# Performance work log

Measured on AMD Instinct MI355X. Metric: run time of the kernel, lower is better.

## Reference

```python
import jax, jax.numpy as jnp
import numpy as np


def reverse_padded(tokens, lengths):
    # reverse each row within its valid length; padding stays in place
    B, T = tokens.shape
    t = jnp.arange(T)[None, :]
    L = lengths[:, None]
    idx = jnp.where(t < L, L - 1 - t, t)
    return jnp.take_along_axis(tokens, idx, axis=1)


def lstm_layer(x, lengths, Wih, Whh, bih, bhh):
    # x: [T, B, I]; emulates packed LSTM: padded steps output zeros, state frozen
    T, B, _ = x.shape
    H = Whh.shape[1]
    xW = jnp.einsum('tbi,gi->tbg', x, Wih) + bih  # precompute input GEMM [T,B,4H]
    mask = (jnp.arange(T)[:, None] < lengths[None, :]).astype(x.dtype)[:, :, None]

    def step(carry, inp):
        h, c = carry
        xw, m = inp
        gates = xw + h @ Whh.T + bhh
        i, f, g, o = jnp.split(gates, 4, axis=-1)
        i = jax.nn.sigmoid(i); f = jax.nn.sigmoid(f)
        g = jnp.tanh(g); o = jax.nn.sigmoid(o)
        c_new = f * c + i * g
        h_new = o * jnp.tanh(c_new)
        h = m * h_new + (1.0 - m) * h
        c = m * c_new + (1.0 - m) * c
        return (h, c), m * h_new

    h0 = jnp.zeros((B, H), x.dtype)
    (hT, cT), out = jax.lax.scan(step, (h0, h0), (xW, mask))
    return out


def setup_inputs() -> dict:
    key = jax.random.key(0)
    ntoken, ninp, nhid, B, T = 50000, 512, 1024, 64, 512
    ks = jax.random.split(key, 40)
    inp = {}
    inp['input'] = jax.random.randint(ks[0], (B, T), 0, ntoken)
    lens = jnp.sort(jax.random.randint(ks[1], (B,), T // 4, T + 1))[::-1]
    inp['seq_lengths'] = lens.at[0].set(T)
    inp['enc'] = jax.random.uniform(ks[2], (ntoken, ninp), jnp.float32, -0.1, 0.1)
    k = 3
    for d in ('f', 'r'):
        for l in range(2):
            I = ninp if l == 0 else nhid
            s = 1.0 / np.sqrt(nhid)
            inp[f'Wih_{d}{l}'] = jax.random.uniform(ks[k], (4 * nhid, I), jnp.float32, -s, s); k += 1
            inp[f'Whh_{d}{l}'] = jax.random.uniform(ks[k], (4 * nhid, nhid), jnp.float32, -s, s); k += 1
            inp[f'bih_{d}{l}'] = jax.random.uniform(ks[k], (4 * nhid,), jnp.float32, -s, s); k += 1
            inp[f'bhh_{d}{l}'] = jax.random.uniform(ks[k], (4 * nhid,), jnp.float32, -s, s); k += 1
    return inp


def reference(input, seq_lengths, enc,
              Wih_f0, Whh_f0, bih_f0, bhh_f0,
              Wih_f1, Whh_f1, bih_f1, bhh_f1,
              Wih_r0, Whh_r0, bih_r0, bhh_r0,
              Wih_r1, Whh_r1, bih_r1, bhh_r1):
    # eval-mode Elmo forward (all dropouts identity)
    input_rev = reverse_padded(input, seq_lengths)
    emb = enc[input].transpose(1, 0, 2)          # [T,B,ninp]
    emb_rev = enc[input_rev].transpose(1, 0, 2)  # [T,B,ninp]
    h_f = lstm_layer(emb, seq_lengths, Wih_f0, Whh_f0, bih_f0, bhh_f0)
    h_f = lstm_layer(h_f, seq_lengths, Wih_f1, Whh_f1, bih_f1, bhh_f1)
    h_r = lstm_layer(emb_rev, seq_lengths, Wih_r0, Whh_r0, bih_r0, bhh_r0)
    h_r = lstm_layer(h_r, seq_lengths, Wih_r1, Whh_r1, bih_r1, bhh_r1)
    return jnp.concatenate([h_f, h_r], axis=-1)  # [T,B,2*nhid]
```

## Files before the change

kernel.cpp:

```cpp
#include <hip/hip_runtime.h>

#define TT 512
#define BB 64
#define NI 512
#define NH 1024
#define NG 4096

using bf16x8 = __attribute__((ext_vector_type(8))) __bf16;
using f32x4  = __attribute__((ext_vector_type(4))) float;

typedef __attribute__((address_space(3))) char       lds_char;
typedef const __attribute__((address_space(1))) char glb_char;

static __device__ __forceinline__ unsigned short f2bf(float f) {
  unsigned int u = __float_as_uint(f);
  u += 0x7fffu + ((u >> 16) & 1u);
  return (unsigned short)(u >> 16);
}

__global__ void prep_layer(const float* __restrict__ Wih, const float* __restrict__ Whh,
                           const float* __restrict__ bih, const float* __restrict__ bhh,
                           unsigned short* __restrict__ Wx, unsigned short* __restrict__ Wh,
                           float* __restrict__ bias, int Kx) {
  long nx = (long)NG * Kx;
  long nh = (long)NG * NH;
  long total = nx + nh + NG;
  for (long i = (long)blockIdx.x * blockDim.x + threadIdx.x; i < total;
       i += (long)gridDim.x * blockDim.x) {
    if (i < nx) {
      int p = (int)(i / Kx); int k = (int)(i - (long)p * Kx);
      int orig = (p & 3) * NH + (p >> 2);
      Wx[i] = f2bf(Wih[(long)orig * Kx + k]);
    } else if (i < nx + nh) {
      long j = i - nx;
      int p = (int)(j / NH); int k = (int)(j - (long)p * NH);
      int orig = (p & 3) * NH + (p >> 2);
      Wh[j] = f2bf(Whh[(long)orig * NH + k]);
    } else {
      int p = (int)(i - nx - nh);
      int orig = (p & 3) * NH + (p >> 2);
      bias[p] = bih[orig] + bhh[orig];
    }
  }
}

__global__ void prep_emb(const int* __restrict__ tok, const int* __restrict__ lens,
                         const float* __restrict__ enc,
                         unsigned short* __restrict__ embf, unsigned short* __restrict__ embr) {
  int row = blockIdx.x;
  int t = row / BB, b = row - (row / BB) * BB;
  int L = lens[b];
  int tf = tok[b * TT + t];
  int ir = (t < L) ? (L - 1 - t) : t;
  int tr_ = tok[b * TT + ir];
  int i = threadIdx.x;
  float4 vf = *(const float4*)(enc + (long)tf * NI + i * 4);
  float4 vr = *(const float4*)(enc + (long)tr_ * NI + i * 4);
  ushort4 of = make_ushort4(f2bf(vf.x), f2bf(vf.y), f2bf(vf.z), f2bf(vf.w));
  ushort4 orr = make_ushort4(f2bf(vr.x), f2bf(vr.y), f2bf(vr.z), f2bf(vr.w));
  *(ushort4*)(embf + (long)row * NI + i * 4) = of;
  *(ushort4*)(embr + (long)row * NI + i * 4) = orr;
}

struct KP {
  const int* lens;
  const unsigned short* emb[2];
  const unsigned short* Wx[4];
  const unsigned short* Wh[4];
  const float* bias[4];
  unsigned short* hist[4];
  unsigned int* slots;
  float* out;
};

static __device__ __forceinline__ void poll_comb(const unsigned int* slots, int g,
                                                 int v, int layer, int t) {
  const int lane = threadIdx.x & 63;
  const bool nown = (t > 0) && (lane < 8);
  const bool nprev = layer && (lane >= 8) && (lane < 16);
  const unsigned int* p = slots;
  unsigned tgt = 0u;
  if (nown)  { p = slots + (size_t)(g * 64 + v * 8 + lane) * 8;            tgt = (unsigned)t; }
  if (nprev) { p = slots + (size_t)((g - 1) * 64 + v * 8 + (lane - 8)) * 8; tgt = (unsigned)(t + 1); }
  for (;;) {
    unsigned val = __hip_atomic_load(p, __ATOMIC_RELAXED, __HIP_MEMORY_SCOPE_AGENT);
    if (__all((int)(val >= tgt))) break;
    __builtin_amdgcn_s_sleep(1);
  }
  asm volatile("" ::: "memory");
}

__global__ void __launch_bounds__(512, 2) lstm_main(KP P) {
  __shared__ f32x4 red[8 * 16 * 64];
  __shared__ unsigned short hrep[64][16];
  __shared__ float hrep2[64][17];
  const int tid = threadIdx.x, lane = tid & 63, wave = tid >> 6;
  const int v = wave;
  const int wg = blockIdx.x, g = wg >> 6, wl = wg & 63;
  const int dir = g >> 1, layer = g & 1;
  const int ln = lane & 15, kg = lane >> 4;

  bf16x8 wh[16], wx[16];
  const int row0 = wl * 64;
  {
    const unsigned short* Wh = P.Wh[g];
#pragma unroll
    for (int mt = 0; mt < 4; ++mt) {
      const unsigned short* p = Wh + (long)(row0 + mt * 16 + ln) * NH + v * 128 + kg * 8;
#pragma unroll
      for (int kk = 0; kk < 4; ++kk) wh[mt * 4 + kk] = *(const bf16x8*)(p + kk * 32);
    }
    const unsigned short* Wxp = P.Wx[g];
    if (layer) {
#pragma unroll
      for (int mt = 0; mt < 4; ++mt) {
        const unsigned short* p = Wxp + (long)(row0 + mt * 16 + ln) * NH + v * 128 + kg * 8;
#pragma unroll
        for (int kk = 0; kk < 4; ++kk) wx[mt * 4 + kk] = *(const bf16x8*)(p + kk * 32);
      }
    } else {
#pragma unroll
      for (int mt = 0; mt < 4; ++mt) {
        const unsigned short* p = Wxp + (long)(row0 + mt * 16 + ln) * NI + v * 64 + kg * 8;
#pragma unroll
        for (int kk = 0; kk < 2; ++kk) wx[mt * 2 + kk] = *(const bf16x8*)(p + kk * 32);
      }
#pragma unroll
      for (int i = 8; i < 16; ++i) wx[i] = (bf16x8)0;
    }
  }
#pragma unroll
  for (int i = 0; i < 16; ++i) {
    asm volatile("" : "+v"(reinterpret_cast<f32x4&>(wh[i])));
    asm volatile("" : "+v"(reinterpret_cast<f32x4&>(wx[i])));
  }

  unsigned short* hist = P.hist[g];
  const unsigned short* xprev = layer ? (const unsigned short*)P.hist[g - 1] : nullptr;
  const unsigned short* xemb = P.emb[dir];

  const int i0 = wave * 2;
  const int coll = (i0 >> 2) * 4 + kg;
  const int b0 = (i0 & 3) * 16 + ln;
  const int b1 = ((i0 + 1) & 3) * 16 + ln;
  const f32x4 bias_v = *(const f32x4*)(P.bias[g] + (wl * 16 + coll) * 4);
  const int L0 = P.lens[b0], L1 = P.lens[b1];
  float c0 = 0.f, c1 = 0.f;

  const int sr = wave * 8 + (lane >> 3);
  const int sc = lane & 7;

  lds_char* lslice = (lds_char*)((char*)red + v * 16384);

  for (int t = 0; t < TT; ++t) {
    f32x4 acc[16];
#pragma unroll
    for (int i = 0; i < 16; ++i) { f32x4 z = {0.f, 0.f, 0.f, 0.f}; acc[i] = z; }

    if (t > 0 || layer) poll_comb(P.slots, g, v, layer, t);

    if (t > 0) {
      const char* gsrc = (const char*)(hist + (size_t)(t - 1) * 65536 + (size_t)v * 8192);
#pragma unroll
      for (int c = 0; c < 16; ++c) {
        __builtin_amdgcn_global_load_lds(
            (glb_char*)(gsrc + c * 1024 + lane * 16),
            (lds_char*)(lslice + c * 1024), 16, 0, 0);
      }
    }

    if (layer) {
      const unsigned short* pb = xprev + (size_t)t * 65536 +
          (size_t)(v * 8 + (kg >> 1)) * 1024 + ln * 16 + (kg & 1) * 8;
      bf16x8 bx[4][4];
#pragma unroll
      for (int kk = 0; kk < 4; ++kk)
#pragma unroll
        for (int nt = 0; nt < 4; ++nt)
          bx[kk][nt] = *(const bf16x8*)(pb + kk * 2048 + nt * 256);
#pragma unroll
      for (int kk = 0; kk < 4; ++kk)
#pragma unroll
        for (int mt = 0; mt < 4; ++mt)
#pragma unroll
          for (int nt = 0; nt < 4; ++nt)
            acc[mt * 4 + nt] = __builtin_amdgcn_mfma_f32_16x16x32_bf16(
                wx[mt * 4 + kk], bx[kk][nt], acc[mt * 4 + nt], 0, 0, 0);
    } else {
      const unsigned short* pb = xemb + ((size_t)t * BB + ln) * NI + v * 64 + kg * 8;
      bf16x8 bx[2][4];
#pragma unroll
      for (int kk = 0; kk < 2; ++kk)
#pragma unroll
        for (int nt = 0; nt < 4; ++nt)
          bx[kk][nt] = *(const bf16x8*)(pb + kk * 32 + (size_t)nt * 16 * NI);
#pragma unroll
      for (int kk = 0; kk < 2; ++kk)
#pragma unroll
        for (int mt = 0; mt < 4; ++mt)
#pragma unroll
          for (int nt = 0; nt < 4; ++nt)
            acc[mt * 4 + nt] = __builtin_amdgcn_mfma_f32_16x16x32_bf16(
                wx[mt * 2 + kk], bx[kk][nt], acc[mt * 4 + nt], 0, 0, 0);
    }

    if (t > 0) {
      asm volatile("s_waitcnt vmcnt(0)" ::: "memory");
      __builtin_amdgcn_sched_barrier(0);
      const char* ls = (const char*)red + v * 16384 +
                       (kg >> 1) * 2048 + ln * 32 + (kg & 1) * 16;
      bf16x8 bh[2][4];
#pragma unroll
      for (int nt = 0; nt < 4; ++nt)
        bh[0][nt] = *(const bf16x8*)(ls + nt * 512);
#pragma unroll
      for (int kk = 0; kk < 4; ++kk) {
        if (kk < 3) {
#pragma unroll
          for (int nt = 0; nt < 4; ++nt)
            bh[(kk + 1) & 1][nt] = *(const bf16x8*)(ls + (kk + 1) * 4096 + nt * 512);
        }
#pragma unroll
        for (int mt = 0; mt < 4; ++mt)
#pragma unroll
          for (int nt = 0; nt < 4; ++nt)
            acc[mt * 4 + nt] = __builtin_amdgcn_mfma_f32_16x16x32_bf16(
                wh[mt * 4 + kk], bh[kk & 1][nt], acc[mt * 4 + nt], 0, 0, 0);
      }
      asm volatile("s_waitcnt lgkmcnt(0)" ::: "memory");
      __builtin_amdgcn_sched_barrier(0);
    }

#pragma unroll
    for (int i = 0; i < 16; ++i) red[(wave * 16 + i) * 64 + lane] = acc[i];
    __syncthreads();

#pragma unroll
    for (int u = 0; u < 2; ++u) {
      const int i = i0 + u;
      f32x4 gs = bias_v;
#pragma unroll
      for (int w2 = 0; w2 < 8; ++w2) gs += red[(w2 * 16 + i) * 64 + lane];
      float iv = 1.f / (1.f + __expf(-gs[0]));
      float fv = 1.f / (1.f + __expf(-gs[1]));
      float gv = 1.f - 2.f / (1.f + __expf(2.f * gs[2]));
      float og = 1.f / (1.f + __expf(-gs[3]));
      float cp = u ? c1 : c0;
      float cn = fv * cp + iv * gv;
      if (u) c1 = cn; else c0 = cn;
      float tc = 1.f - 2.f / (1.f + __expf(2.f * cn));
      float hn = og * tc;
      const int Lx = u ? L1 : L0;
      const int bx = u ? b1 : b0;
      float outv = (t < Lx) ? hn : 0.f;
      hrep[bx][coll] = f2bf(outv);
      if (layer) hrep2[bx][coll] = outv;
    }
    __syncthreads();

    {
      unsigned vv = ((const unsigned*)hrep)[tid];
      __hip_atomic_store(
          (unsigned*)(hist + (size_t)t * 65536 + (size_t)wl * 1024) + tid,
          vv, __ATOMIC_RELAXED, __HIP_MEMORY_SCOPE_AGENT);
    }
    asm volatile("s_waitcnt vmcnt(0)" ::: "memory");
    __syncthreads();
    if (tid == 0)
      __hip_atomic_store(P.slots + (size_t)wg * 8, (unsigned)(t + 1),
                         __ATOMIC_RELAXED, __HIP_MEMORY_SCOPE_AGENT);
    if (layer) {
#pragma unroll
      for (int u = 0; u < 2; ++u) {
        float vv = hrep2[sr][sc + u * 8];
        __builtin_nontemporal_store(
            vv, &P.out[(long)(t * BB + sr) * 2048 + dir * NH + wl * 16 + sc + u * 8]);
      }
    }
  }
}

extern "C" void kernel_launch(void* const* d_in, const int* in_sizes, int n_in,
                              void* d_out, int out_size, void* d_ws, size_t ws_size,
                              hipStream_t stream) {
  (void)in_sizes; (void)n_in; (void)out_size; (void)ws_size;
  const int* input = (const int*)d_in[0];
  const int* lens  = (const int*)d_in[1];
  const float* enc = (const float*)d_in[2];
  const float* Wih[4] = {(const float*)d_in[3],  (const float*)d_in[7],
                         (const float*)d_in[11], (const float*)d_in[15]};
  const float* Whh[4] = {(const float*)d_in[4],  (const float*)d_in[8],
                         (const float*)d_in[12], (const float*)d_in[16]};
  const float* bih[4] = {(const float*)d_in[5],  (const float*)d_in[9],
                         (const float*)d_in[13], (const float*)d_in[17]};
  const float* bhh[4] = {(const float*)d_in[6],  (const float*)d_in[10],
                         (const float*)d_in[14], (const float*)d_in[18]};

  char* ws = (char*)d_ws;
  size_t off = 0;
  auto carve = [&](size_t bytes) -> char* {
    char* p = ws + off;
    off += (bytes + 255) & ~(size_t)255;
    return p;
  };
  unsigned short* emb[2];
  emb[0] = (unsigned short*)carve((size_t)TT * BB * NI * 2);
  emb[1] = (unsigned short*)carve((size_t)TT * BB * NI * 2);
  unsigned short* hist[4];
  for (int g = 0; g < 4; ++g)
    hist[g] = (unsigned short*)carve((size_t)TT * BB * NH * 2);
  unsigned short* Wx[4]; unsigned short* Wh[4]; float* bias[4];
  for (int li = 0; li < 4; ++li) {
    int Kx = (li & 1) ? NH : NI;
    Wx[li]   = (unsigned short*)carve((size_t)NG * Kx * 2);
    Wh[li]   = (unsigned short*)carve((size_t)NG * NH * 2);
    bias[li] = (float*)carve((size_t)NG * 4);
  }
  unsigned int* slots = (unsigned int*)carve(256 * 32);

  hipMemsetAsync(slots, 0, 256 * 32, stream);
  for (int li = 0; li < 4; ++li) {
    int Kx = (li & 1) ? NH : NI;
    prep_layer<<<2048, 256, 0, stream>>>(Wih[li], Whh[li], bih[li], bhh[li],
                                         Wx[li], Wh[li], bias[li], Kx);
  }
  prep_emb<<<TT * BB, 128, 0, stream>>>(input, lens, enc, emb[0], emb[1]);

  KP p;
  p.lens = lens;
  p.emb[0] = emb[0]; p.emb[1] = emb[1];
  for (int li = 0; li < 4; ++li) {
    p.Wx[li] = Wx[li]; p.Wh[li] = Wh[li]; p.bias[li] = bias[li]; p.hist[li] = hist[li];
  }
  p.slots = slots;
  p.out = (float*)d_out;

  void* args[] = {&p};
  hipLaunchCooperativeKernel(lstm_main, dim3(256), dim3(512), args, 0, stream);
}
```

Baseline: 3.934 ms.

## Remap gate elementwise to thread-per-batch pairs, drop LDS staging, prefetch embedding

The gate activation step is remapped so each thread handles one batch row and two adjacent hidden columns. This lets it pack the bf16 h values and the fp32 outputs directly into stores, which removes the hrep/hrep2 LDS buffers and one __syncthreads per timestep. For layer 0, the next timestep's embedding operands are prefetched into registers after the step's signal store, taking the global-load latency off the critical recurrence path. The cost is extra register pressure from the prefetch buffer and a different LDS read pattern during the reduction, which may cause bank conflicts.

```diff
diff --git a/kernel.cpp b/kernel.cpp
--- a/kernel.cpp
+++ b/kernel.cpp
@@ -92,8 +92,6 @@
 
 __global__ void __launch_bounds__(512, 2) lstm_main(KP P) {
   __shared__ f32x4 red[8 * 16 * 64];
-  __shared__ unsigned short hrep[64][16];
-  __shared__ float hrep2[64][17];
   const int tid = threadIdx.x, lane = tid & 63, wave = tid >> 6;
   const int v = wave;
   const int wg = blockIdx.x, g = wg >> 6, wl = wg & 63;
@@ -139,18 +137,26 @@
   const unsigned short* xprev = layer ? (const unsigned short*)P.hist[g - 1] : nullptr;
   const unsigned short* xemb = P.emb[dir];
 
-  const int i0 = wave * 2;
-  const int coll = (i0 >> 2) * 4 + kg;
-  const int b0 = (i0 & 3) * 16 + ln;
-  const int b1 = ((i0 + 1) & 3) * 16 + ln;
-  const f32x4 bias_v = *(const f32x4*)(P.bias[g] + (wl * 16 + coll) * 4);
-  const int L0 = P.lens[b0], L1 = P.lens[b1];
-  float c0 = 0.f, c1 = 0.f;
-
-  const int sr = wave * 8 + (lane >> 3);
-  const int sc = lane & 7;
+  const int eb = tid >> 3;
+  const int c2 = tid & 7;
+  const int rbase = ((c2 >> 1) * 4 + (eb >> 4)) * 64 +
+                    ((2 * c2) & 3) * 16 + (eb & 15);
+  const f32x4 bias0 = *(const f32x4*)(P.bias[g] + (wl * 16 + 2 * c2) * 4);
+  const f32x4 bias1 = *(const f32x4*)(P.bias[g] + (wl * 16 + 2 * c2 + 1) * 4);
+  const int L = P.lens[eb];
+  float cs0 = 0.f, cs1 = 0.f;
 
   lds_char* lslice = (lds_char*)((char*)red + v * 16384);
+
+  bf16x8 pre[8];
+  if (!layer) {
+    const unsigned short* pb = xemb + (size_t)ln * NI + v * 64 + kg * 8;
+#pragma unroll
+    for (int kk = 0; kk < 2; ++kk)
+#pragma unroll
+      for (int nt = 0; nt < 4; ++nt)
+        pre[kk * 4 + nt] = *(const bf16x8*)(pb + kk * 32 + (size_t)nt * 16 * NI);
+  }
 
   for (int t = 0; t < TT; ++t) {
     f32x4 acc[16];
@@ -187,13 +193,6 @@
             acc[mt * 4 + nt] = __builtin_amdgcn_mfma_f32_16x16x32_bf16(
                 wx[mt * 4 + kk], bx[kk][nt], acc[mt * 4 + nt], 0, 0, 0);
     } else {
-      const unsigned short* pb = xemb + ((size_t)t * BB + ln) * NI + v * 64 + kg * 8;
-      bf16x8 bx[2][4];
-#pragma unroll
-      for (int kk = 0; kk < 2; ++kk)
-#pragma unroll
-        for (int nt = 0; nt < 4; ++nt)
-          bx[kk][nt] = *(const bf16x8*)(pb + kk * 32 + (size_t)nt * 16 * NI);
 #pragma unroll
       for (int kk = 0; kk < 2; ++kk)
 #pragma unroll
@@ -201,7 +200,7 @@
 #pragma unroll
           for (int nt = 0; nt < 4; ++nt)
             acc[mt * 4 + nt] = __builtin_amdgcn_mfma_f32_16x16x32_bf16(
-                wx[mt * 2 + kk], bx[kk][nt], acc[mt * 4 + nt], 0, 0, 0);
+                wx[mt * 2 + kk], pre[kk * 4 + nt], acc[mt * 4 + nt], 0, 0, 0);
     }
 
     if (t > 0) {
@@ -235,34 +234,35 @@
     for (int i = 0; i < 16; ++i) red[(wave * 16 + i) * 64 + lane] = acc[i];
     __syncthreads();
 
-#pragma unroll
-    for (int u = 0; u < 2; ++u) {
-      const int i = i0 + u;
-      f32x4 gs = bias_v;
-#pragma unroll
-      for (int w2 = 0; w2 < 8; ++w2) gs += red[(w2 * 16 + i) * 64 + lane];
-      float iv = 1.f / (1.f + __expf(-gs[0]));
-      float fv = 1.f / (1.f + __expf(-gs[1]));
-      float gv = 1.f - 2.f / (1.f + __expf(2.f * gs[2]));
-      float og = 1.f / (1.f + __expf(-gs[3]));
-      float cp = u ? c1 : c0;
-      float cn = fv * cp + iv * gv;
-      if (u) c1 = cn; else c0 = cn;
-      float tc = 1.f - 2.f / (1.f + __expf(2.f * cn));
-      float hn = og * tc;
-      const int Lx = u ? L1 : L0;
-      const int bx = u ? b1 : b0;
-      float outv = (t < Lx) ? hn : 0.f;
-      hrep[bx][coll] = f2bf(outv);
-      if (layer) hrep2[bx][coll] = outv;
-    }
-    __syncthreads();
-
+    float ov0, ov1;
     {
-      unsigned vv = ((const unsigned*)hrep)[tid];
+      f32x4 g0 = bias0, g1 = bias1;
+#pragma unroll
+      for (int w2 = 0; w2 < 8; ++w2) {
+        g0 += red[w2 * 1024 + rbase];
+        g1 += red[w2 * 1024 + rbase + 16];
+      }
+      float i0v = 1.f / (1.f + __expf(-g0[0]));
+      float f0v = 1.f / (1.f + __expf(-g0[1]));
+      float g0v = 1.f - 2.f / (1.f + __expf(2.f * g0[2]));
+      float o0v = 1.f / (1.f + __expf(-g0[3]));
+      float i1v = 1.f / (1.f + __expf(-g1[0]));
+      float f1v = 1.f / (1.f + __expf(-g1[1]));
+      float g1v = 1.f - 2.f / (1.f + __expf(2.f * g1[2]));
+      float o1v = 1.f / (1.f + __expf(-g1[3]));
+      float cn0 = f0v * cs0 + i0v * g0v;
+      float cn1 = f1v * cs1 + i1v * g1v;
+      bool m = t < L;
+      cs0 = m ? cn0 : cs0;
+      cs1 = m ? cn1 : cs1;
+      float hn0 = o0v * (1.f - 2.f / (1.f + __expf(2.f * cn0)));
+      float hn1 = o1v * (1.f - 2.f / (1.f + __expf(2.f * cn1)));
+      ov0 = m ? hn0 : 0.f;
+      ov1 = m ? hn1 : 0.f;
+      unsigned hd = (unsigned)f2bf(ov0) | ((unsigned)f2bf(ov1) << 16);
       __hip_atomic_store(
           (unsigned*)(hist + (size_t)t * 65536 + (size_t)wl * 1024) + tid,
-          vv, __ATOMIC_RELAXED, __HIP_MEMORY_SCOPE_AGENT);
+          hd, __ATOMIC_RELAXED, __HIP_MEMORY_SCOPE_AGENT);
     }
     asm volatile("s_waitcnt vmcnt(0)" ::: "memory");
     __syncthreads();
@@ -270,12 +270,17 @@
       __hip_atomic_store(P.slots + (size_t)wg * 8, (unsigned)(t + 1),
                          __ATOMIC_RELAXED, __HIP_MEMORY_SCOPE_AGENT);
     if (layer) {
-#pragma unroll
-      for (int u = 0; u < 2; ++u) {
-        float vv = hrep2[sr][sc + u * 8];
-        __builtin_nontemporal_store(
-            vv, &P.out[(long)(t * BB + sr) * 2048 + dir * NH + wl * 16 + sc + u * 8]);
-      }
+      union { float f[2]; double d; } U;
+      U.f[0] = ov0; U.f[1] = ov1;
+      __builtin_nontemporal_store(
+          U.d, (double*)(P.out + (long)(t * BB + eb) * 2048 + dir * NH + wl * 16 + 2 * c2));
+    } else if (t + 1 < TT) {
+      const unsigned short* pb = xemb + ((size_t)(t + 1) * BB + ln) * NI + v * 64 + kg * 8;
+#pragma unroll
+      for (int kk = 0; kk < 2; ++kk)
+#pragma unroll
+        for (int nt = 0; nt < 4; ++nt)
+          pre[kk * 4 + nt] = *(const bf16x8*)(pb + kk * 32 + (size_t)nt * 16 * NI);
     }
   }
 }
```

New measurement: 4.960 ms. 1.26x slower.
